# Performance work log

Hardware: AMD Instinct MI355X
Metric: run time of the kernel (lower is better)

The kernel has to match this reference:

```python
import jax, jax.numpy as jnp
import numpy as np
import math

E = 256          # embed_dims
H = 8            # num_heads
ITER = 2         # iterative steps
PC_RANGE = (-140.8, -40.0, -3.0, 140.8, 40.0, 1.0)


def sine_embed(pos, num_feats):
    # pos: (..., 3) in (0,1); returns (..., 3*num_feats), per-coord interleaved sin/cos
    scale = 2.0 * math.pi
    i = jnp.arange(num_feats, dtype=jnp.float32)
    dim_t = 10000.0 ** (2.0 * jnp.floor(i / 2.0) / num_feats)
    p = pos[..., None] * scale / dim_t                      # (..., 3, F)
    emb = jnp.stack([jnp.sin(p[..., 0::2]), jnp.cos(p[..., 1::2])], axis=-1)
    emb = emb.reshape(p.shape[:-1] + (num_feats,))          # (..., 3, F)
    return emb.reshape(pos.shape[:-1] + (3 * num_feats,))


def mha(q, k, v, Wi, bi, Wo, bo, n_heads):
    # torch nn.MultiheadAttention math, seq-first layout: q (L,N,C), k/v (M,N,C)
    L, N, C = q.shape
    D = C // n_heads
    qp = (q @ Wi[:C].T + bi[:C]).reshape(L, N, n_heads, D)
    kp = (k @ Wi[C:2 * C].T + bi[C:2 * C]).reshape(k.shape[0], N, n_heads, D)
    vp = (v @ Wi[2 * C:].T + bi[2 * C:]).reshape(v.shape[0], N, n_heads, D)
    scores = jnp.einsum('lnhd,mnhd->nhlm', qp, kp) / math.sqrt(D)
    attn = jax.nn.softmax(scores, axis=-1)
    o = jnp.einsum('nhlm,mnhd->lnhd', attn, vp).reshape(L, N, C)
    return o @ Wo.T + bo


def setup_inputs() -> dict:
    key = jax.random.key(0)
    ks = jax.random.split(key, 12)
    Q, TOT, B, LMAX = 2048, 40, 8, 5
    s = 0.02
    return {
        'x': jax.random.normal(ks[0], (Q, TOT, E), jnp.float32),
        'reference_points': jax.random.uniform(ks[1], (TOT, Q, 3), jnp.float32),
        'pairwise_t_matrix': jax.random.normal(ks[2], (B, LMAX, LMAX, 4, 4), jnp.float32),
        'record_len': np.full((B,), 5, dtype=np.int64),
        'in_proj_w': jax.random.normal(ks[3], (3 * E, E), jnp.float32) * s,
        'in_proj_b': jnp.zeros((3 * E,), jnp.float32),
        'out_w': jax.random.normal(ks[4], (E, E), jnp.float32) * s,
        'out_b': jnp.zeros((E,), jnp.float32),
        'bev_w1': jax.random.normal(ks[5], (E, 3 * E), jnp.float32) * s,
        'bev_b1': jnp.zeros((E,), jnp.float32),
        'bev_w2': jax.random.normal(ks[6], (E, E), jnp.float32) * s,
        'bev_b2': jnp.zeros((E,), jnp.float32),
    }


def reference(x, reference_points, pairwise_t_matrix, in_proj_w, in_proj_b,
              out_w, out_b, bev_w1, bev_b1, bev_w2, bev_b2, record_len):
    rl = np.asarray(record_len)
    offsets = np.concatenate([[0], np.cumsum(rl)]).astype(int)
    lo = jnp.asarray(PC_RANGE[:3], jnp.float32)
    hi = jnp.asarray(PC_RANGE[3:], jnp.float32)

    x_cav = jnp.transpose(x, (1, 0, 2))                    # (total_cav, Q, C)
    ref = reference_points * (hi - lo) + lo                # un-normalize to pc_range

    outs = []
    for b in range(len(rl)):
        s, e = offsets[b], offsets[b + 1]
        n = e - s
        b_x = x_cav[s:e]                                   # (n, Q, C)
        if n == 1:
            outs.append(b_x)
            continue
        b_ref = ref[s:e]                                   # (n, Q, 3)
        t_ego = pairwise_t_matrix[b, :n, 0]                # (n, 4, 4) transform-to-ego
        homo = jnp.concatenate([b_ref, jnp.ones(b_ref.shape[:-1] + (1,), b_ref.dtype)], axis=-1)
        trans = jax.nn.sigmoid(jnp.einsum('nij,nqj->nqi', t_ego, homo)[..., :3])
        pe = sine_embed(trans, E)                          # (n, Q, 3E)
        bev = jax.nn.relu(pe @ bev_w1.T + bev_b1) @ bev_w2.T + bev_b2  # (n, Q, C)

        ego = b_x[0:1]
        neigh = b_x[1:]                                    # (n-1, Q, C)
        kk = neigh + bev[1:]
        for _ in range(ITER):
            q = jnp.broadcast_to(ego, neigh.shape)
            o = q + mha(q, kk, neigh, in_proj_w, in_proj_b, out_w, out_b, H)
            ego = jnp.sum(o, axis=0, keepdims=True)
        outs.append(jnp.concatenate([ego, neigh], axis=0))

    out = jnp.concatenate(outs, axis=0)                    # (total_cav, Q, C)
    return jnp.transpose(out, (1, 0, 2))                   # (Q, total_cav, C)
```

## Files before the change

kernel.cpp:

```cpp
#include <hip/hip_runtime.h>
#include <cstdint>
#include <cstddef>

typedef __bf16 bf16;
typedef __attribute__((ext_vector_type(8))) __bf16 bf16x8;
typedef __attribute__((ext_vector_type(4))) float f32x4;
typedef __attribute__((ext_vector_type(4))) unsigned int u32x4;

#define QN 2048

__device__ __forceinline__ float sigmoidf_(float v) { return 1.0f / (1.0f + __expf(-v)); }

__device__ __forceinline__ bf16x8 cvt8(const float* p) {
  const f32x4* p4 = (const f32x4*)p;
  f32x4 lo = p4[0], hi = p4[1];
  bf16x8 r;
#pragma unroll
  for (int j = 0; j < 4; ++j) { r[j] = (bf16)lo[j]; r[j + 4] = (bf16)hi[j]; }
  return r;
}

__device__ __forceinline__ void load_lds16(const bf16* g, bf16* l) {
  __builtin_amdgcn_global_load_lds(
      (const __attribute__((address_space(1))) void*)g,
      (__attribute__((address_space(3))) void*)l, 16, 0, 0);
}

__global__ __launch_bounds__(256) void copy_ker(const u32x4* __restrict__ in,
                                                u32x4* __restrict__ out, int n) {
  int i = blockIdx.x * 256 + threadIdx.x;
  if (i < n) out[i] = in[i];
}

__global__ __launch_bounds__(256) void cvtw_ker(const float* __restrict__ ipw,
                                                const float* __restrict__ ow,
                                                const float* __restrict__ w1,
                                                const float* __restrict__ w2,
                                                bf16* __restrict__ wb) {
  int e = (blockIdx.x * 256 + threadIdx.x) * 8;
  const float* src; int off;
  if (e < 196608)      { src = ipw; off = e; }
  else if (e < 262144) { src = ow;  off = e - 196608; }
  else if (e < 458752) { src = w1;  off = e - 262144; }
  else                 { src = w2;  off = e - 458752; }
  *(bf16x8*)(wb + e) = cvt8(src + off);
}

template <int AMODE, int EPI, int KDIM>
__global__ __launch_bounds__(256) void gemm_ker(
    const bf16* __restrict__ A, const float* __restrict__ Af,
    const bf16* __restrict__ W, const float* __restrict__ bias,
    const float* __restrict__ x, const float* __restrict__ rp,
    const float* __restrict__ pm, const float* __restrict__ egoPrev,
    bf16* __restrict__ outB, float* __restrict__ outF) {
  __shared__ bf16 As[128][40];
  __shared__ bf16 Bs[128][32];

  const int tid = threadIdx.x;
  const int bidm = blockIdx.x >> 1;
  const int bidn = blockIdx.x & 1;
  const int rowBase = bidm << 7;
  const int colBase = bidn << 7;

  const int wave = tid >> 6, lane = tid & 63;
  const int m16 = lane & 15, quad = lane >> 4;
  const int wr = wave >> 1, wc = wave & 1;

  const int sRow = tid >> 1, sHalf = tid & 1;
  const int rgA = rowBase + sRow;

  const float* afp = nullptr;
  float tr0 = 0.f, tr1 = 0.f, tr2 = 0.f;
  if constexpr (AMODE == 1) {
    int b = rgA >> 13, j = (rgA >> 11) & 3, q = rgA & 2047;
    int t = b * 5 + 1 + j;
    const float* rpp = rp + ((size_t)t * QN + q) * 3;
    float r0 = rpp[0] * 281.6f - 140.8f;
    float r1 = rpp[1] * 80.0f - 40.0f;
    float r2 = rpp[2] * 4.0f - 3.0f;
    const float* T = pm + (size_t)t * 80;
    tr0 = sigmoidf_(T[0] * r0 + T[1] * r1 + T[2] * r2 + T[3]);
    tr1 = sigmoidf_(T[4] * r0 + T[5] * r1 + T[6] * r2 + T[7]);
    tr2 = sigmoidf_(T[8] * r0 + T[9] * r1 + T[10] * r2 + T[11]);
  } else if constexpr (AMODE == 2) {
    int b = rgA >> 13, j = (rgA >> 11) & 3, q = rgA & 2047;
    afp = x + (((size_t)q * 40 + b * 5 + 1 + j) << 8);
  } else if constexpr (AMODE == 3) {
    int b = rgA >> 11, q = rgA & 2047;
    afp = x + (((size_t)q * 40 + b * 5) << 8);
  } else if constexpr (AMODE == 4) {
    afp = Af + (size_t)rgA * 256;
  }

  const bf16* wsrc = W + (size_t)(colBase + (wave << 5) + (lane >> 2)) * KDIM + ((lane & 3) << 3);
  bf16* bdst0 = &Bs[(wave << 5)][0];
  bf16* bdst1 = &Bs[(wave << 5) + 16][0];

  f32x4 acc[4][4] = {};

  for (int k0 = 0; k0 < KDIM; k0 += 32) {
    load_lds16(wsrc + k0, bdst0);
    load_lds16(wsrc + (size_t)16 * KDIM + k0, bdst1);

    bf16x8 a0, a1;
    if constexpr (AMODE == 1) {
      int c = k0 >> 8;
      float tc = (c == 0) ? tr0 : (c == 1 ? tr1 : tr2);
      int l0 = (k0 & 255) + (sHalf << 4);
#pragma unroll
      for (int jj = 0; jj < 8; ++jj) {
        int l = l0 + jj, ti = l >> 1;
        float freq = exp2f((float)ti * -0.10381025296522975f);
        float ang = tc * 6.283185307179586f * freq;
        a0[jj] = (bf16)((l & 1) ? __cosf(ang) : __sinf(ang));
      }
#pragma unroll
      for (int jj = 0; jj < 8; ++jj) {
        int l = l0 + 8 + jj, ti = l >> 1;
        float freq = exp2f((float)ti * -0.10381025296522975f);
        float ang = tc * 6.283185307179586f * freq;
        a1[jj] = (bf16)((l & 1) ? __cosf(ang) : __sinf(ang));
      }
    } else if constexpr (AMODE == 0) {
      const bf16* ap = A + (size_t)rgA * KDIM + k0 + (sHalf << 4);
      a0 = ((const bf16x8*)ap)[0];
      a1 = ((const bf16x8*)ap)[1];
    } else {
      const float* fp = afp + k0 + (sHalf << 4);
      a0 = cvt8(fp);
      a1 = cvt8(fp + 8);
    }
    *(bf16x8*)(&As[sRow][sHalf << 4]) = a0;
    *(bf16x8*)(&As[sRow][(sHalf << 4) + 8]) = a1;
    __syncthreads();

    bf16x8 afr[4], bfr[4];
#pragma unroll
    for (int mt = 0; mt < 4; ++mt)
      afr[mt] = *(const bf16x8*)(&As[(wr << 6) + (mt << 4) + m16][quad << 3]);
#pragma unroll
    for (int nt = 0; nt < 4; ++nt)
      bfr[nt] = *(const bf16x8*)(&Bs[(wc << 6) + (nt << 4) + m16][quad << 3]);
#pragma unroll
    for (int mt = 0; mt < 4; ++mt)
#pragma unroll
      for (int nt = 0; nt < 4; ++nt)
        acc[mt][nt] = __builtin_amdgcn_mfma_f32_16x16x32_bf16(
            afr[mt], bfr[nt], acc[mt][nt], 0, 0, 0);
    __syncthreads();
  }

#pragma unroll
  for (int mt = 0; mt < 4; ++mt) {
#pragma unroll
    for (int nt = 0; nt < 4; ++nt) {
      const int col = colBase + (wc << 6) + (nt << 4) + m16;
      const float bv = bias[col];
#pragma unroll
      for (int rg = 0; rg < 4; ++rg) {
        const int r = rowBase + (wr << 6) + (mt << 4) + (quad << 2) + rg;
        float v = acc[mt][nt][rg] + bv;
        if constexpr (EPI == 0) {
          outB[(size_t)r * 256 + col] = (bf16)fmaxf(v, 0.0f);
        } else if constexpr (EPI == 1) {
          int b = r >> 13, j = (r >> 11) & 3, q = r & 2047;
          v += x[(((size_t)q * 40 + b * 5 + 1 + j) << 8) + col];
          outB[(size_t)r * 256 + col] = (bf16)v;
        } else if constexpr (EPI == 2) {
          outB[(size_t)r * 256 + col] = (bf16)v;
        } else if constexpr (EPI == 3) {
          int b = r >> 11, q = r & 2047;
          float xe = x[(((size_t)q * 40 + b * 5) << 8) + col];
          outF[(size_t)r * 256 + col] = 4.0f * (xe + v);
        } else if constexpr (EPI == 4) {
          int b = r >> 11, q = r & 2047;
          float e1 = egoPrev[(size_t)r * 256 + col];
          outF[(((size_t)q * 40 + b * 5) << 8) + col] = 4.0f * (e1 + v);
        }
      }
    }
  }
}

__global__ __launch_bounds__(256) void attn_ker(const bf16* __restrict__ qp,
                                                const bf16* __restrict__ kp,
                                                const bf16* __restrict__ vp,
                                                bf16* __restrict__ o) {
  int p = blockIdx.x * 256 + threadIdx.x;
  int h = p & 7;
  int re = p >> 3;
  int b = re >> 11;
  int q = re & 2047;
  const bf16x8* qpv = (const bf16x8*)(qp + ((size_t)re << 8) + h * 32);
  float qv[32];
#pragma unroll
  for (int i = 0; i < 4; ++i) {
    bf16x8 t = qpv[i];
#pragma unroll
    for (int j = 0; j < 8; ++j) qv[i * 8 + j] = (float)t[j];
  }
  size_t base = ((size_t)(b * 4) * QN + q) * 256 + h * 32;
  float s[4];
#pragma unroll
  for (int m = 0; m < 4; ++m) {
    const bf16x8* kv = (const bf16x8*)(kp + base + (size_t)m * (QN * 256));
    float a = 0.f;
#pragma unroll
    for (int i = 0; i < 4; ++i) {
      bf16x8 t = kv[i];
#pragma unroll
      for (int j = 0; j < 8; ++j) a += qv[i * 8 + j] * (float)t[j];
    }
    s[m] = a * 0.17677669529663687f;
  }
  float mx = fmaxf(fmaxf(s[0], s[1]), fmaxf(s[2], s[3]));
  float e0 = __expf(s[0] - mx), e1 = __expf(s[1] - mx);
  float e2 = __expf(s[2] - mx), e3 = __expf(s[3] - mx);
  float inv = 1.0f / (e0 + e1 + e2 + e3);
  float w[4] = {e0 * inv, e1 * inv, e2 * inv, e3 * inv};
  float ov[32] = {};
#pragma unroll
  for (int m = 0; m < 4; ++m) {
    const bf16x8* vv = (const bf16x8*)(vp + base + (size_t)m * (QN * 256));
#pragma unroll
    for (int i = 0; i < 4; ++i) {
      bf16x8 t = vv[i];
#pragma unroll
      for (int j = 0; j < 8; ++j) ov[i * 8 + j] += w[m] * (float)t[j];
    }
  }
  bf16x8* op = (bf16x8*)(o + ((size_t)re << 8) + h * 32);
#pragma unroll
  for (int i = 0; i < 4; ++i) {
    bf16x8 t;
#pragma unroll
    for (int j = 0; j < 8; ++j) t[j] = (bf16)ov[i * 8 + j];
    op[i] = t;
  }
}

extern "C" void kernel_launch(void* const* d_in, const int* in_sizes, int n_in,
                              void* d_out, int out_size, void* d_ws, size_t ws_size,
                              hipStream_t stream) {
  (void)n_in; (void)out_size; (void)ws_size;
  const float* x   = (const float*)d_in[0];
  const float* rp  = (const float*)d_in[1];
  const float* pm  = (const float*)d_in[2];
  const int wbase = (in_sizes[3] == 8) ? 4 : 3;
  const float* ipw = (const float*)d_in[wbase + 0];
  const float* ipb = (const float*)d_in[wbase + 1];
  const float* ow  = (const float*)d_in[wbase + 2];
  const float* obv = (const float*)d_in[wbase + 3];
  const float* w1  = (const float*)d_in[wbase + 4];
  const float* b1  = (const float*)d_in[wbase + 5];
  const float* w2  = (const float*)d_in[wbase + 6];
  const float* b2  = (const float*)d_in[wbase + 7];
  float* out = (float*)d_out;
  char* ws = (char*)d_ws;

  bf16* h    = (bf16*)(ws + 0);
  bf16* kk   = (bf16*)(ws + 33554432);
  bf16* kp   = (bf16*)(ws + 0);
  bf16* vp   = (bf16*)(ws + 67108864);
  bf16* qp   = (bf16*)(ws + 33554432);
  bf16* oo   = (bf16*)(ws + 41943040);
  float* egoF = (float*)(ws + 50331648);
  bf16* wb   = (bf16*)(ws + 100663296);
  const bf16* wq  = wb;
  const bf16* wk  = wb + 65536;
  const bf16* wv  = wb + 131072;
  const bf16* owb = wb + 196608;
  const bf16* w1b = wb + 262144;
  const bf16* w2b = wb + 458752;

  cvtw_ker<<<256, 256, 0, stream>>>(ipw, ow, w1, w2, wb);
  copy_ker<<<20480, 256, 0, stream>>>((const u32x4*)x, (u32x4*)out, 5242880);
  gemm_ker<1, 0, 768><<<1024, 256, 0, stream>>>(nullptr, nullptr, w1b, b1, x, rp, pm, nullptr, h, nullptr);
  gemm_ker<0, 1, 256><<<1024, 256, 0, stream>>>(h, nullptr, w2b, b2, x, rp, pm, nullptr, kk, nullptr);
  gemm_ker<0, 2, 256><<<1024, 256, 0, stream>>>(kk, nullptr, wk, ipb + 256, x, rp, pm, nullptr, kp, nullptr);
  gemm_ker<2, 2, 256><<<1024, 256, 0, stream>>>(nullptr, nullptr, wv, ipb + 512, x, rp, pm, nullptr, vp, nullptr);
  gemm_ker<3, 2, 256><<<256, 256, 0, stream>>>(nullptr, nullptr, wq, ipb, x, rp, pm, nullptr, qp, nullptr);
  attn_ker<<<512, 256, 0, stream>>>(qp, kp, vp, oo);
  gemm_ker<0, 3, 256><<<256, 256, 0, stream>>>(oo, nullptr, owb, obv, x, rp, pm, nullptr, nullptr, egoF);
  gemm_ker<4, 2, 256><<<256, 256, 0, stream>>>(nullptr, egoF, wq, ipb, x, rp, pm, nullptr, qp, nullptr);
  attn_ker<<<512, 256, 0, stream>>>(qp, kp, vp, oo);
  gemm_ker<0, 4, 256><<<256, 256, 0, stream>>>(oo, nullptr, owb, obv, x, rp, pm, egoF, nullptr, out);
}
```

Baseline: 386.2 us.

## Fold bev second layer into key projection and cheapen sine embedding

Precomputes a combined weight Wk·W2 and bias so that the key projection reads relu(h) and the neighbour features as one K=512 GEMM. This removes the separate bev_w2 GEMM and the kk intermediate buffer. The sine embedding now uses the hardware revolution-based sin/cos and a multiplicative frequency recurrence instead of a per-element exp2, and the output copy skips the ego rows that are later overwritten. Rounding the combined weight to bf16 and the recurrence drift could change numerics slightly.

```diff
diff --git a/kernel.cpp b/kernel.cpp
--- a/kernel.cpp
+++ b/kernel.cpp
@@ -9,6 +9,14 @@
 
 #define QN 2048
 
+#if __has_builtin(__builtin_amdgcn_sinf)
+#define SIN_REV(x) __builtin_amdgcn_sinf(x)
+#define COS_REV(x) __builtin_amdgcn_cosf(x)
+#else
+#define SIN_REV(x) __sinf((x) * 6.283185307179586f)
+#define COS_REV(x) __cosf((x) * 6.283185307179586f)
+#endif
+
 __device__ __forceinline__ float sigmoidf_(float v) { return 1.0f / (1.0f + __expf(-v)); }
 
 __device__ __forceinline__ bf16x8 cvt8(const float* p) {
@@ -29,7 +37,10 @@
 __global__ __launch_bounds__(256) void copy_ker(const u32x4* __restrict__ in,
                                                 u32x4* __restrict__ out, int n) {
   int i = blockIdx.x * 256 + threadIdx.x;
-  if (i < n) out[i] = in[i];
+  if (i >= n) return;
+  int t = (i >> 6) % 40;
+  if ((t % 5) == 0) return;
+  out[i] = in[i];
 }
 
 __global__ __launch_bounds__(256) void cvtw_ker(const float* __restrict__ ipw,
@@ -44,6 +55,31 @@
   else if (e < 458752) { src = w1;  off = e - 262144; }
   else                 { src = w2;  off = e - 458752; }
   *(bf16x8*)(wb + e) = cvt8(src + off);
+}
+
+__global__ __launch_bounds__(256) void wcomb_ker(const float* __restrict__ ipw,
+                                                 const float* __restrict__ ipb,
+                                                 const float* __restrict__ w2f,
+                                                 const float* __restrict__ b2f,
+                                                 bf16* __restrict__ Wc,
+                                                 float* __restrict__ bkf) {
+  __shared__ float row[256];
+  __shared__ float red[256];
+  const int j = blockIdx.x, l = threadIdx.x;
+  row[l] = ipw[65536 + j * 256 + l];
+  __syncthreads();
+  float acc = 0.f;
+#pragma unroll 4
+  for (int m = 0; m < 256; ++m) acc += row[m] * w2f[m * 256 + l];
+  Wc[(size_t)j * 512 + l] = (bf16)acc;
+  Wc[(size_t)j * 512 + 256 + l] = (bf16)row[l];
+  red[l] = row[l] * b2f[l];
+  __syncthreads();
+  for (int s = 128; s > 0; s >>= 1) {
+    if (l < s) red[l] += red[l + s];
+    __syncthreads();
+  }
+  if (l == 0) bkf[j] = ipb[256 + j] + red[0];
 }
 
 template <int AMODE, int EPI, int KDIM>
@@ -82,7 +118,7 @@
     tr0 = sigmoidf_(T[0] * r0 + T[1] * r1 + T[2] * r2 + T[3]);
     tr1 = sigmoidf_(T[4] * r0 + T[5] * r1 + T[6] * r2 + T[7]);
     tr2 = sigmoidf_(T[8] * r0 + T[9] * r1 + T[10] * r2 + T[11]);
-  } else if constexpr (AMODE == 2) {
+  } else if constexpr (AMODE == 2 || AMODE == 5) {
     int b = rgA >> 13, j = (rgA >> 11) & 3, q = rgA & 2047;
     afp = x + (((size_t)q * 40 + b * 5 + 1 + j) << 8);
   } else if constexpr (AMODE == 3) {
@@ -106,25 +142,36 @@
     if constexpr (AMODE == 1) {
       int c = k0 >> 8;
       float tc = (c == 0) ? tr0 : (c == 1 ? tr1 : tr2);
-      int l0 = (k0 & 255) + (sHalf << 4);
-#pragma unroll
-      for (int jj = 0; jj < 8; ++jj) {
-        int l = l0 + jj, ti = l >> 1;
-        float freq = exp2f((float)ti * -0.10381025296522975f);
-        float ang = tc * 6.283185307179586f * freq;
-        a0[jj] = (bf16)((l & 1) ? __cosf(ang) : __sinf(ang));
+      int ti0 = ((k0 & 255) + (sHalf << 4)) >> 1;
+      float freq = exp2f((float)ti0 * -0.10381025296522975f);
+#pragma unroll
+      for (int p = 0; p < 4; ++p) {
+        float ang = tc * freq;
+        a0[2 * p]     = (bf16)SIN_REV(ang);
+        a0[2 * p + 1] = (bf16)COS_REV(ang);
+        freq *= 0.93057204092467f;
       }
 #pragma unroll
-      for (int jj = 0; jj < 8; ++jj) {
-        int l = l0 + 8 + jj, ti = l >> 1;
-        float freq = exp2f((float)ti * -0.10381025296522975f);
-        float ang = tc * 6.283185307179586f * freq;
-        a1[jj] = (bf16)((l & 1) ? __cosf(ang) : __sinf(ang));
+      for (int p = 0; p < 4; ++p) {
+        float ang = tc * freq;
+        a1[2 * p]     = (bf16)SIN_REV(ang);
+        a1[2 * p + 1] = (bf16)COS_REV(ang);
+        freq *= 0.93057204092467f;
       }
     } else if constexpr (AMODE == 0) {
       const bf16* ap = A + (size_t)rgA * KDIM + k0 + (sHalf << 4);
       a0 = ((const bf16x8*)ap)[0];
       a1 = ((const bf16x8*)ap)[1];
+    } else if constexpr (AMODE == 5) {
+      if (k0 < 256) {
+        const bf16* ap = A + ((size_t)rgA << 8) + k0 + (sHalf << 4);
+        a0 = ((const bf16x8*)ap)[0];
+        a1 = ((const bf16x8*)ap)[1];
+      } else {
+        const float* fp = afp + (k0 - 256) + (sHalf << 4);
+        a0 = cvt8(fp);
+        a1 = cvt8(fp + 8);
+      }
     } else {
       const float* fp = afp + k0 + (sHalf << 4);
       a0 = cvt8(fp);
@@ -259,25 +306,24 @@
   char* ws = (char*)d_ws;
 
   bf16* h    = (bf16*)(ws + 0);
-  bf16* kk   = (bf16*)(ws + 33554432);
-  bf16* kp   = (bf16*)(ws + 0);
+  bf16* qp   = (bf16*)(ws + 0);
+  bf16* oo   = (bf16*)(ws + 8388608);
+  bf16* kp   = (bf16*)(ws + 33554432);
   bf16* vp   = (bf16*)(ws + 67108864);
-  bf16* qp   = (bf16*)(ws + 33554432);
-  bf16* oo   = (bf16*)(ws + 41943040);
-  float* egoF = (float*)(ws + 50331648);
-  bf16* wb   = (bf16*)(ws + 100663296);
+  float* egoF = (float*)(ws + 100663296);
+  bf16* wb   = (bf16*)(ws + 117440512);
+  bf16* Wc   = (bf16*)(ws + 118489088);
+  float* bkf = (float*)(ws + 118751232);
   const bf16* wq  = wb;
-  const bf16* wk  = wb + 65536;
   const bf16* wv  = wb + 131072;
   const bf16* owb = wb + 196608;
   const bf16* w1b = wb + 262144;
-  const bf16* w2b = wb + 458752;
 
   cvtw_ker<<<256, 256, 0, stream>>>(ipw, ow, w1, w2, wb);
+  wcomb_ker<<<256, 256, 0, stream>>>(ipw, ipb, w2, b2, Wc, bkf);
   copy_ker<<<20480, 256, 0, stream>>>((const u32x4*)x, (u32x4*)out, 5242880);
   gemm_ker<1, 0, 768><<<1024, 256, 0, stream>>>(nullptr, nullptr, w1b, b1, x, rp, pm, nullptr, h, nullptr);
-  gemm_ker<0, 1, 256><<<1024, 256, 0, stream>>>(h, nullptr, w2b, b2, x, rp, pm, nullptr, kk, nullptr);
-  gemm_ker<0, 2, 256><<<1024, 256, 0, stream>>>(kk, nullptr, wk, ipb + 256, x, rp, pm, nullptr, kp, nullptr);
+  gemm_ker<5, 2, 512><<<1024, 256, 0, stream>>>(h, nullptr, Wc, bkf, x, rp, pm, nullptr, kp, nullptr);
   gemm_ker<2, 2, 256><<<1024, 256, 0, stream>>>(nullptr, nullptr, wv, ipb + 512, x, rp, pm, nullptr, vp, nullptr);
   gemm_ker<3, 2, 256><<<256, 256, 0, stream>>>(nullptr, nullptr, wq, ipb, x, rp, pm, nullptr, qp, nullptr);
   attn_ker<<<512, 256, 0, stream>>>(qp, kp, vp, oo);
```

After: 382.7 us. No clear change (-0.9%).
